# Kernel optimization log

Measured on AMD Instinct MI355X. Metric: run time of the kernel, lower is better.

## Reference

```python
import jax, jax.numpy as jnp
import numpy as np
import math

DIM = 1024; NH = 16; HD = 64; RANK = 512
E = 8; TOPK = 2; EH = 512
THETA = 10000.0; EPS = 1e-6
B = 2; T = 2048


def setup_inputs():
    key = jax.random.key(0)
    ks = jax.random.split(key, 12)
    s = 0.02
    return {
        "x": jax.random.normal(ks[0], (B, T, DIM), jnp.float32),
        "attn_norm_w": jnp.ones((DIM,), jnp.float32),
        "ffn_norm_w": jnp.ones((DIM,), jnp.float32),
        "q_norm_w": jnp.ones((HD,), jnp.float32),
        "k_norm_w": jnp.ones((HD,), jnp.float32),
        "wq": jax.random.normal(ks[1], (NH * HD, DIM), jnp.float32) * s,
        "wkv_down": jax.random.normal(ks[2], (RANK, DIM), jnp.float32) * s,
        "wkv_up": jax.random.normal(ks[3], (2 * NH * HD, RANK), jnp.float32) * s,
        "wo": jax.random.normal(ks[4], (DIM, NH * HD), jnp.float32) * s,
        "gate_w": jax.random.normal(ks[5], (E, DIM), jnp.float32) * s,
        "shared_w1": jax.random.normal(ks[6], (EH, DIM), jnp.float32) * s,
        "shared_w2": jax.random.normal(ks[7], (DIM, EH), jnp.float32) * s,
        "expert_w1": jax.random.normal(ks[8], (E, EH, DIM), jnp.float32) * s,
        "expert_w2": jax.random.normal(ks[9], (E, DIM, EH), jnp.float32) * s,
    }


def rmsnorm(x, w):
    var = jnp.mean(x * x, axis=-1, keepdims=True)
    return x * jax.lax.rsqrt(var + EPS) * w


def rope(x, cos, sin):
    # x: [B,T,H,HD]; pairs are (even, odd) along last dim. cos/sin: [T,1,HD//2]
    xr = x.reshape(*x.shape[:-1], HD // 2, 2)
    a, b = xr[..., 0], xr[..., 1]
    out = jnp.stack([a * cos - b * sin, a * sin + b * cos], axis=-1)
    return out.reshape(x.shape)


def _block(x, attn_norm_w, ffn_norm_w, q_norm_w, k_norm_w,
           wq, wkv_down, wkv_up, wo, gate_w,
           shared_w1, shared_w2, expert_w1, expert_w2):
    Bb, Tt, C = x.shape
    # ---- MLA attention ----
    h_in = rmsnorm(x, attn_norm_w)
    xq = jnp.einsum('btd,ed->bte', h_in, wq).reshape(Bb, Tt, NH, HD)
    latent = jnp.einsum('btd,rd->btr', h_in, wkv_down)
    kv = jnp.einsum('btr,er->bte', latent, wkv_up).reshape(Bb, Tt, 2, NH, HD)
    xk, xv = kv[:, :, 0], kv[:, :, 1]
    xq = rmsnorm(xq, q_norm_w)
    xk = rmsnorm(xk, k_norm_w)
    # RoPE tables
    inv = 1.0 / (THETA ** (jnp.arange(0, HD, 2, dtype=jnp.float32) / HD))  # [HD/2]
    ang = jnp.arange(Tt, dtype=jnp.float32)[:, None] * inv[None, :]       # [T,HD/2]
    cos = jnp.cos(ang)[:, None, :]
    sin = jnp.sin(ang)[:, None, :]
    xq = rope(xq, cos, sin)
    xk = rope(xk, cos, sin)
    scale = 1.0 / math.sqrt(HD)
    scores = jnp.einsum('bqhd,bkhd->bhqk', xq, xk) * scale
    causal = jnp.tril(jnp.ones((Tt, Tt), dtype=bool))
    scores = jnp.where(causal, scores, jnp.finfo(scores.dtype).min)
    attn = jax.nn.softmax(scores, axis=-1)
    attn_out = jnp.einsum('bhqk,bkhd->bqhd', attn, xv).reshape(Bb, Tt, C)
    attn_out = jnp.einsum('bte,de->btd', attn_out, wo)
    h = x + attn_out  # dropout p=0.0 -> identity

    # ---- DeepSeekMoE ----
    xm = rmsnorm(h, ffn_norm_w).reshape(-1, C)  # [N,D]
    shared = jnp.einsum('nh,dh->nd', jax.nn.silu(jnp.einsum('nd,hd->nh', xm, shared_w1)), shared_w2)
    logits = jnp.einsum('nd,ed->ne', xm, gate_w)
    probs = jax.nn.softmax(logits, axis=-1)
    tkw, tki = jax.lax.top_k(probs, TOPK)
    tkw = tkw / jnp.sum(tkw, axis=-1, keepdims=True)
    aux_loss = jnp.sum(jnp.mean(probs, axis=0) * jnp.mean(logits, axis=0)) * E
    # combine weights per expert: [N,E]
    combine = jnp.einsum('nk,nke->ne', tkw, jax.nn.one_hot(tki, E, dtype=tkw.dtype))
    hidden = jax.nn.silu(jnp.einsum('nd,ehd->neh', xm, expert_w1))  # [N,E,EH]
    yexp = jnp.einsum('neh,edh->ned', hidden, expert_w2)            # [N,E,D]
    routed = jnp.einsum('ne,ned->nd', combine, yexp)
    moe_out = (shared + routed).reshape(Bb, Tt, C)
    out = h + moe_out
    return out, aux_loss


def reference(x, attn_norm_w, ffn_norm_w, q_norm_w, k_norm_w,
              wq, wkv_down, wkv_up, wo, gate_w,
              shared_w1, shared_w2, expert_w1, expert_w2):
    return _block(x, attn_norm_w, ffn_norm_w, q_norm_w, k_norm_w,
                  wq, wkv_down, wkv_up, wo, gate_w,
                  shared_w1, shared_w2, expert_w1, expert_w2)
```

## Files before the change

kernel.cpp:

```cpp
#include <hip/hip_runtime.h>
#include <math.h>

#define DIMC 1024
#define NHEADS 16
#define HDC 64
#define RANKC 512
#define NEXP 8
#define EHC 512
#define SEQC 2048
#define NBATCH 2
#define NTOK (NBATCH * SEQC)
#define EPSF 1e-6f

typedef unsigned short u16;
using bf16x8 = __attribute__((ext_vector_type(8))) short;
using f32x4 = __attribute__((ext_vector_type(4))) float;

__device__ inline u16 f2bf(float f) {
    unsigned int u = __float_as_uint(f);
    u += 0x7fff + ((u >> 16) & 1);
    return (u16)(u >> 16);
}
__device__ inline float bf2f(u16 u) { return __uint_as_float(((unsigned int)u) << 16); }

__device__ inline void gld16(const void* g, void* l) {
    __builtin_amdgcn_global_load_lds(
        (const __attribute__((address_space(1))) unsigned int*)g,
        (__attribute__((address_space(3))) unsigned int*)l, 16, 0, 0);
}

__global__ __launch_bounds__(256) void convall_k(
    const float* __restrict__ wq, const float* __restrict__ wkvd,
    const float* __restrict__ wkvu, const float* __restrict__ wo,
    const float* __restrict__ sw1, const float* __restrict__ sw2,
    const float* __restrict__ ew1, const float* __restrict__ ew2,
    u16* __restrict__ wqkvd_h, u16* __restrict__ wqkvd_l,
    u16* __restrict__ wkvu_h, u16* __restrict__ wkvu_l,
    u16* __restrict__ wo_h, u16* __restrict__ wo_l,
    u16* __restrict__ sw1_b, u16* __restrict__ sw2_b,
    u16* __restrict__ ew1_b, u16* __restrict__ ew2_b) {
    size_t f = ((size_t)blockIdx.x * 256 + threadIdx.x) * 4;
    const float* src;
    u16* dh;
    u16* dl = nullptr;
    size_t local;
    if (f < 1048576) { src = wq; dh = wqkvd_h; dl = wqkvd_l; local = f; }
    else if (f < 1572864) { src = wkvd; dh = wqkvd_h + 1048576; dl = wqkvd_l + 1048576; local = f - 1048576; }
    else if (f < 2621440) { src = wkvu; dh = wkvu_h; dl = wkvu_l; local = f - 1572864; }
    else if (f < 3670016) { src = wo; dh = wo_h; dl = wo_l; local = f - 2621440; }
    else if (f < 4194304) { src = sw1; dh = sw1_b; local = f - 3670016; }
    else if (f < 4718592) { src = sw2; dh = sw2_b; local = f - 4194304; }
    else if (f < 8912896) { src = ew1; dh = ew1_b; local = f - 4718592; }
    else { src = ew2; dh = ew2_b; local = f - 8912896; }
    float4 a = *(const float4*)(src + local);
    ushort4 h = make_ushort4(f2bf(a.x), f2bf(a.y), f2bf(a.z), f2bf(a.w));
    *(ushort4*)(dh + local) = h;
    if (dl) {
        ushort4 lo = make_ushort4(f2bf(a.x - bf2f(h.x)), f2bf(a.y - bf2f(h.y)),
                                  f2bf(a.z - bf2f(h.z)), f2bf(a.w - bf2f(h.w)));
        *(ushort4*)(dl + local) = lo;
    }
}

template <bool SPLIT, bool WF32>
__global__ __launch_bounds__(256) void rmsnorm_k(const float* __restrict__ x,
                                                 const float* __restrict__ w,
                                                 u16* __restrict__ oh,
                                                 u16* __restrict__ ol,
                                                 float* __restrict__ of) {
    int row = blockIdx.x;
    const float* xr = x + (size_t)row * DIMC;
    int base = threadIdx.x * 4;
    float4 xv = *(const float4*)(xr + base);
    float ss = xv.x * xv.x + xv.y * xv.y + xv.z * xv.z + xv.w * xv.w;
#pragma unroll
    for (int off = 32; off; off >>= 1) ss += __shfl_down(ss, off);
    __shared__ float sred[4];
    int wid = threadIdx.x >> 6, lane = threadIdx.x & 63;
    if (lane == 0) sred[wid] = ss;
    __syncthreads();
    float tot = sred[0] + sred[1] + sred[2] + sred[3];
    float sc = rsqrtf(tot * (1.0f / DIMC) + EPSF);
    float4 wv = *(const float4*)(w + base);
    float o0 = xv.x * sc * wv.x, o1 = xv.y * sc * wv.y;
    float o2 = xv.z * sc * wv.z, o3 = xv.w * sc * wv.w;
    ushort4 h = make_ushort4(f2bf(o0), f2bf(o1), f2bf(o2), f2bf(o3));
    size_t ob = (size_t)row * DIMC + base;
    *(ushort4*)(oh + ob) = h;
    if (SPLIT) {
        ushort4 lo = make_ushort4(f2bf(o0 - bf2f(h.x)), f2bf(o1 - bf2f(h.y)),
                                  f2bf(o2 - bf2f(h.z)), f2bf(o3 - bf2f(h.w)));
        *(ushort4*)(ol + ob) = lo;
    }
    if (WF32) *(float4*)(of + ob) = make_float4(o0, o1, o2, o3);
}

template <int EPI>
__global__ __launch_bounds__(256) void gemm_sp(const u16* __restrict__ Ah,
                                               const u16* __restrict__ Al,
                                               const u16* __restrict__ Bh,
                                               const u16* __restrict__ Bl,
                                               float* __restrict__ Cf,
                                               u16* __restrict__ Ch,
                                               u16* __restrict__ Cl,
                                               const float* __restrict__ res,
                                               int M, int K) {
    __shared__ u16 AsH[128 * 32], AsL[128 * 32];
    __shared__ u16 BsH[64 * 32], BsL[64 * 32];
    int m0 = blockIdx.x * 64, n0 = blockIdx.y * 128;
    int t = threadIdx.x;
    int w = t >> 6, l = t & 63;
    int wr = w >> 1, wc = w & 1;
    f32x4 acc[4][2];
#pragma unroll
    for (int i = 0; i < 4; i++)
#pragma unroll
        for (int j = 0; j < 2; j++) acc[i][j] = {0.f, 0.f, 0.f, 0.f};
    int lr = t >> 2, lcb = (t & 3) * 8;
    size_t aoff = (size_t)(n0 + lr) * K + lcb;
    size_t boff = (size_t)(m0 + lr) * K + lcb;
    u16* lAH = AsH + t * 8;
    u16* lAL = AsL + t * 8;
    u16* lBH = BsH + t * 8;
    u16* lBL = BsL + t * 8;
    int arow = l & 15, kblk = (l >> 4) * 8;
    for (int k0 = 0; k0 < K; k0 += 32) {
        if (k0) __syncthreads();
        gld16(Ah + aoff + k0, lAH);
        gld16(Ah + aoff + k0 + (size_t)64 * K, lAH + 2048);
        gld16(Al + aoff + k0, lAL);
        gld16(Al + aoff + k0 + (size_t)64 * K, lAL + 2048);
        gld16(Bh + boff + k0, lBH);
        gld16(Bl + boff + k0, lBL);
        __syncthreads();
        bf16x8 ah[4], al[4], bh[2], bl[2];
#pragma unroll
        for (int i = 0; i < 4; i++) {
            int ar = (wr * 64 + i * 16 + arow) * 32 + kblk;
            ah[i] = *(bf16x8*)(AsH + ar);
            al[i] = *(bf16x8*)(AsL + ar);
        }
#pragma unroll
        for (int j = 0; j < 2; j++) {
            int br = (wc * 32 + j * 16 + arow) * 32 + kblk;
            bh[j] = *(bf16x8*)(BsH + br);
            bl[j] = *(bf16x8*)(BsL + br);
        }
#pragma unroll
        for (int i = 0; i < 4; i++)
#pragma unroll
            for (int j = 0; j < 2; j++) {
                acc[i][j] = __builtin_amdgcn_mfma_f32_16x16x32_bf16(ah[i], bh[j], acc[i][j], 0, 0, 0);
                acc[i][j] = __builtin_amdgcn_mfma_f32_16x16x32_bf16(ah[i], bl[j], acc[i][j], 0, 0, 0);
                acc[i][j] = __builtin_amdgcn_mfma_f32_16x16x32_bf16(al[i], bh[j], acc[i][j], 0, 0, 0);
            }
    }
    int crow = (l >> 4) * 4, ccol = l & 15;
#pragma unroll
    for (int i = 0; i < 4; i++) {
#pragma unroll
        for (int r = 0; r < 4; r++) {
            int n = n0 + wr * 64 + i * 16 + crow + r;
#pragma unroll
            for (int j = 0; j < 2; j++) {
                int mc = m0 + wc * 32 + j * 16 + ccol;
                float vv = acc[i][j][r];
                if (EPI == 0 || EPI == 1) {
                    size_t idx = (size_t)n * M + mc;
                    if (EPI == 1) vv += res[idx];
                    Cf[idx] = vv;
                } else {
                    if (mc < 1024) {
                        Cf[(size_t)n * 1024 + mc] = vv;
                    } else {
                        size_t idx = (size_t)n * 512 + (mc - 1024);
                        u16 hi = f2bf(vv);
                        Ch[idx] = hi;
                        Cl[idx] = f2bf(vv - bf2f(hi));
                    }
                }
            }
        }
    }
}

template <int EPI>
__global__ __launch_bounds__(256) void gemm_bf(const u16* __restrict__ A,
                                               const u16* __restrict__ B,
                                               float* __restrict__ Cf,
                                               u16* __restrict__ Cb,
                                               const float* __restrict__ res,
                                               const u16* __restrict__ yx,
                                               const float* __restrict__ tw,
                                               int M, int K) {
    __shared__ u16 As[128 * 32];
    __shared__ u16 Bs[64 * 32];
    int m0 = blockIdx.x * 64, n0 = blockIdx.y * 128;
    int t = threadIdx.x;
    int w = t >> 6, l = t & 63;
    int wr = w >> 1, wc = w & 1;
    f32x4 acc[4][2];
#pragma unroll
    for (int i = 0; i < 4; i++)
#pragma unroll
        for (int j = 0; j < 2; j++) acc[i][j] = {0.f, 0.f, 0.f, 0.f};
    int lr = t >> 2, lcb = (t & 3) * 8;
    const u16* ga = A + (size_t)(n0 + lr) * K + lcb;
    const u16* gb = B + (size_t)(m0 + lr) * K + lcb;
    u16* lA = As + t * 8;
    u16* lB = Bs + t * 8;
    int arow = l & 15, kblk = (l >> 4) * 8;
    for (int k0 = 0; k0 < K; k0 += 32) {
        if (k0) __syncthreads();
        gld16(ga + k0, lA);
        gld16(ga + k0 + (size_t)64 * K, lA + 2048);
        gld16(gb + k0, lB);
        __syncthreads();
        bf16x8 af[4], bfr[2];
#pragma unroll
        for (int i = 0; i < 4; i++)
            af[i] = *(bf16x8*)(As + (wr * 64 + i * 16 + arow) * 32 + kblk);
#pragma unroll
        for (int j = 0; j < 2; j++)
            bfr[j] = *(bf16x8*)(Bs + (wc * 32 + j * 16 + arow) * 32 + kblk);
#pragma unroll
        for (int i = 0; i < 4; i++)
#pragma unroll
            for (int j = 0; j < 2; j++)
                acc[i][j] = __builtin_amdgcn_mfma_f32_16x16x32_bf16(af[i], bfr[j], acc[i][j], 0, 0, 0);
    }
    int crow = (l >> 4) * 4, ccol = l & 15;
#pragma unroll
    for (int i = 0; i < 4; i++) {
#pragma unroll
        for (int r = 0; r < 4; r++) {
            int n = n0 + wr * 64 + i * 16 + crow + r;
#pragma unroll
            for (int j = 0; j < 2; j++) {
                int mc = m0 + wc * 32 + j * 16 + ccol;
                float vv = acc[i][j][r];
                size_t idx = (size_t)n * M + mc;
                if (EPI == 3) {
                    float y0 = bf2f(yx[(size_t)(2 * n) * 1024 + mc]);
                    float y1 = bf2f(yx[(size_t)(2 * n + 1) * 1024 + mc]);
                    Cf[idx] = vv + res[idx] + tw[2 * n] * y0 + tw[2 * n + 1] * y1;
                } else {
                    vv = vv / (1.0f + __expf(-vv));
                    Cb[idx] = f2bf(vv);
                }
            }
        }
    }
}

__global__ __launch_bounds__(256) void qknorm_rope_k(const float* __restrict__ q,
                                                     const float* __restrict__ kv,
                                                     const float* __restrict__ qw,
                                                     const float* __restrict__ kw,
                                                     u16* __restrict__ qhi, u16* __restrict__ qlo,
                                                     u16* __restrict__ khi, u16* __restrict__ klo) {
    int bid = blockIdx.x * 4 + (threadIdx.x >> 6);
    int head = bid & (NHEADS - 1);
    int n = bid >> 4;
    int pos = n & (SEQC - 1);
    int lane = threadIdx.x & 63;
    int i = lane >> 1;
    float inv = powf(10000.0f, -(float)(2 * i) * (1.0f / HDC));
    float ang = (float)pos * inv;
    float cs = cosf(ang), sn = sinf(ang);
    size_t off = (size_t)n * DIMC + head * HDC + lane;
    {
        float v = q[off];
        float ss = v * v;
#pragma unroll
        for (int o2 = 32; o2; o2 >>= 1) ss += __shfl_down(ss, o2);
        ss = __shfl(ss, 0);
        float sc = rsqrtf(ss * (1.0f / HDC) + EPSF);
        v = v * sc * qw[lane];
        float partner = __shfl_xor(v, 1);
        float outv = (lane & 1) ? (partner * sn + v * cs) : (v * cs - partner * sn);
        outv *= 0.125f;
        u16 hi = f2bf(outv);
        qhi[off] = hi;
        qlo[off] = f2bf(outv - bf2f(hi));
    }
    {
        float v = kv[(size_t)n * 2048 + head * HDC + lane];
        float ss = v * v;
#pragma unroll
        for (int o2 = 32; o2; o2 >>= 1) ss += __shfl_down(ss, o2);
        ss = __shfl(ss, 0);
        float sc = rsqrtf(ss * (1.0f / HDC) + EPSF);
        v = v * sc * kw[lane];
        float partner = __shfl_xor(v, 1);
        float outv = (lane & 1) ? (partner * sn + v * cs) : (v * cs - partner * sn);
        u16 hi = f2bf(outv);
        khi[off] = hi;
        klo[off] = f2bf(outv - bf2f(hi));
    }
}

__global__ __launch_bounds__(256) void transp_k(const float* __restrict__ kv,
                                                u16* __restrict__ vthi,
                                                u16* __restrict__ vtlo) {
    __shared__ float T[64][68];
    int j0 = blockIdx.x * 64, head = blockIdx.y, b = blockIdx.z;
    int t = threadIdx.x;
    int jr = t >> 2, c0 = (t & 3) * 16;
    const float* src = kv + ((size_t)(b * SEQC + j0 + jr)) * 2048 + 1024 + head * HDC + c0;
#pragma unroll
    for (int u = 0; u < 4; u++) {
        float4 v4 = *(const float4*)(src + u * 4);
        T[c0 + u * 4 + 0][jr] = v4.x;
        T[c0 + u * 4 + 1][jr] = v4.y;
        T[c0 + u * 4 + 2][jr] = v4.z;
        T[c0 + u * 4 + 3][jr] = v4.w;
    }
    __syncthreads();
    int d = t >> 2, jb = (t & 3) * 16;
    size_t obase = ((size_t)((b * NHEADS + head) * HDC + d)) * SEQC + j0 + jb;
#pragma unroll
    for (int u = 0; u < 4; u++) {
        float f0 = T[d][jb + u * 4 + 0], f1 = T[d][jb + u * 4 + 1];
        float f2 = T[d][jb + u * 4 + 2], f3 = T[d][jb + u * 4 + 3];
        ushort4 h = make_ushort4(f2bf(f0), f2bf(f1), f2bf(f2), f2bf(f3));
        ushort4 lo = make_ushort4(f2bf(f0 - bf2f(h.x)), f2bf(f1 - bf2f(h.y)),
                                  f2bf(f2 - bf2f(h.z)), f2bf(f3 - bf2f(h.w)));
        *(ushort4*)(vthi + obase + u * 4) = h;
        *(ushort4*)(vtlo + obase + u * 4) = lo;
    }
}

__device__ __forceinline__ void attn_tile(const bf16x8 (&qh)[2], const bf16x8 (&ql)[2],
                                          f32x4 (&O)[4], float (&mrow)[4], float (&lrow)[4],
                                          const u16* KHs, const u16* KLs,
                                          const u16* VHs, const u16* VLs,
                                          u16* myPH, u16* myPL,
                                          int la, int lg, int w, bool diag) {
    f32x4 S[4];
    __builtin_amdgcn_s_setprio(1);
#pragma unroll
    for (int ct = 0; ct < 4; ct++) {
        int row = ct * 16 + la;
        int sw = (row & 7) << 4;
        int a0 = ((row << 7) + (lg << 4)) ^ sw;
        int a1 = ((row << 7) + 64 + (lg << 4)) ^ sw;
        bf16x8 kh0 = *(const bf16x8*)((const char*)KHs + a0);
        bf16x8 kh1 = *(const bf16x8*)((const char*)KHs + a1);
        bf16x8 kl0 = *(const bf16x8*)((const char*)KLs + a0);
        bf16x8 kl1 = *(const bf16x8*)((const char*)KLs + a1);
        f32x4 s = {0.f, 0.f, 0.f, 0.f};
        s = __builtin_amdgcn_mfma_f32_16x16x32_bf16(qh[0], kh0, s, 0, 0, 0);
        s = __builtin_amdgcn_mfma_f32_16x16x32_bf16(qh[1], kh1, s, 0, 0, 0);
        s = __builtin_amdgcn_mfma_f32_16x16x32_bf16(qh[0], kl0, s, 0, 0, 0);
        s = __builtin_amdgcn_mfma_f32_16x16x32_bf16(qh[1], kl1, s, 0, 0, 0);
        s = __builtin_amdgcn_mfma_f32_16x16x32_bf16(ql[0], kh0, s, 0, 0, 0);
        s = __builtin_amdgcn_mfma_f32_16x16x32_bf16(ql[1], kh1, s, 0, 0, 0);
        S[ct] = s;
    }
    __builtin_amdgcn_s_setprio(0);
    if (diag) {
#pragma unroll
        for (int ct = 0; ct < 4; ct++)
#pragma unroll
            for (int r = 0; r < 4; r++)
                if (ct * 16 + la > w * 16 + lg * 4 + r) S[ct][r] = -1e30f;
    }
    float rmax[4], rsum[4];
#pragma unroll
    for (int r = 0; r < 4; r++)
        rmax[r] = fmaxf(fmaxf(S[0][r], S[1][r]), fmaxf(S[2][r], S[3][r]));
#pragma unroll
    for (int off = 1; off < 16; off <<= 1)
#pragma unroll
        for (int r = 0; r < 4; r++) rmax[r] = fmaxf(rmax[r], __shfl_xor(rmax[r], off));
    float corr[4];
#pragma unroll
    for (int r = 0; r < 4; r++) {
        float mn = fmaxf(mrow[r], rmax[r]);
        corr[r] = __expf(mrow[r] - mn);
        mrow[r] = mn;
        rsum[r] = 0.f;
    }
#pragma unroll
    for (int ct = 0; ct < 4; ct++) {
#pragma unroll
        for (int r = 0; r < 4; r++) {
            float p = __expf(S[ct][r] - mrow[r]);
            rsum[r] += p;
            u16 hi = f2bf(p);
            int pidx = (lg * 4 + r) * 68 + ct * 16 + la;
            myPH[pidx] = hi;
            myPL[pidx] = f2bf(p - bf2f(hi));
        }
    }
#pragma unroll
    for (int off = 1; off < 16; off <<= 1)
#pragma unroll
        for (int r = 0; r < 4; r++) rsum[r] += __shfl_xor(rsum[r], off);
#pragma unroll
    for (int r = 0; r < 4; r++) lrow[r] = lrow[r] * corr[r] + rsum[r];
#pragma unroll
    for (int ct = 0; ct < 4; ct++)
#pragma unroll
        for (int r = 0; r < 4; r++) O[ct][r] *= corr[r];
    asm volatile("s_waitcnt lgkmcnt(0)" ::: "memory");
    __builtin_amdgcn_sched_barrier(0);
    bf16x8 pa0 = *(const bf16x8*)(myPH + la * 68 + lg * 8);
    bf16x8 pa1 = *(const bf16x8*)(myPH + la * 68 + 32 + lg * 8);
    bf16x8 pl0 = *(const bf16x8*)(myPL + la * 68 + lg * 8);
    bf16x8 pl1 = *(const bf16x8*)(myPL + la * 68 + 32 + lg * 8);
    __builtin_amdgcn_s_setprio(1);
#pragma unroll
    for (int ct = 0; ct < 4; ct++) {
        int row = ct * 16 + la;
        int sw = (row & 7) << 4;
        int a0 = ((row << 7) + (lg << 4)) ^ sw;
        int a1 = ((row << 7) + 64 + (lg << 4)) ^ sw;
        bf16x8 vh0 = *(const bf16x8*)((const char*)VHs + a0);
        bf16x8 vh1 = *(const bf16x8*)((const char*)VHs + a1);
        bf16x8 vl0 = *(const bf16x8*)((const char*)VLs + a0);
        bf16x8 vl1 = *(const bf16x8*)((const char*)VLs + a1);
        f32x4 o = O[ct];
        o = __builtin_amdgcn_mfma_f32_16x16x32_bf16(pa0, vh0, o, 0, 0, 0);
        o = __builtin_amdgcn_mfma_f32_16x16x32_bf16(pa1, vh1, o, 0, 0, 0);
        o = __builtin_amdgcn_mfma_f32_16x16x32_bf16(pl0, vh0, o, 0, 0, 0);
        o = __builtin_amdgcn_mfma_f32_16x16x32_bf16(pl1, vh1, o, 0, 0, 0);
        o = __builtin_amdgcn_mfma_f32_16x16x32_bf16(pa0, vl0, o, 0, 0, 0);
        o = __builtin_amdgcn_mfma_f32_16x16x32_bf16(pa1, vl1, o, 0, 0, 0);
        O[ct] = o;
    }
    __builtin_amdgcn_s_setprio(0);
}

__global__ __launch_bounds__(256) void flash_k(const u16* __restrict__ qhi,
                                               const u16* __restrict__ qlo,
                                               const u16* __restrict__ khi,
                                               const u16* __restrict__ klo,
                                               const u16* __restrict__ vthi,
                                               const u16* __restrict__ vtlo,
                                               u16* __restrict__ aoh,
                                               u16* __restrict__ aol) {
    __shared__ u16 KHs[4096], KLs[4096], VHs[4096], VLs[4096];
    __shared__ u16 PH[4][16 * 68], PL[4][16 * 68];
    int pr = blockIdx.x, head = blockIdx.y, b = blockIdx.z;
    int qtA = pr, qtB = 31 - pr;
    int t = threadIdx.x, w = t >> 6, l = t & 63;
    int la = l & 15, lg = l >> 4;
    size_t qoffA = ((size_t)(b * SEQC + qtA * 64 + w * 16 + la)) * DIMC + head * HDC;
    size_t qoffB = ((size_t)(b * SEQC + qtB * 64 + w * 16 + la)) * DIMC + head * HDC;
    bf16x8 qhA[2], qlA[2], qhB[2], qlB[2];
    qhA[0] = *(const bf16x8*)(qhi + qoffA + lg * 8);
    qhA[1] = *(const bf16x8*)(qhi + qoffA + 32 + lg * 8);
    qlA[0] = *(const bf16x8*)(qlo + qoffA + lg * 8);
    qlA[1] = *(const bf16x8*)(qlo + qoffA + 32 + lg * 8);
    qhB[0] = *(const bf16x8*)(qhi + qoffB + lg * 8);
    qhB[1] = *(const bf16x8*)(qhi + qoffB + 32 + lg * 8);
    qlB[0] = *(const bf16x8*)(qlo + qoffB + lg * 8);
    qlB[1] = *(const bf16x8*)(qlo + qoffB + 32 + lg * 8);
    int d0 = t * 16, d1 = 4096 + t * 16;
    int s0 = d0 ^ (((d0 >> 7) & 7) << 4);
    int s1 = d1 ^ (((d1 >> 7) & 7) << 4);
    int r0 = (s0 >> 7) & 63, ir0 = s0 & 127;
    int r1 = (s1 >> 7) & 63, ir1 = s1 & 127;
    size_t kb0 = ((size_t)(b * SEQC + r0) * DIMC + head * HDC) * 2 + ir0;
    size_t kb1 = ((size_t)(b * SEQC + r1) * DIMC + head * HDC) * 2 + ir1;
    size_t vb0 = ((size_t)((b * NHEADS + head) * HDC + r0)) * SEQC * 2 + ir0;
    size_t vb1 = ((size_t)((b * NHEADS + head) * HDC + r1)) * SEQC * 2 + ir1;
    const char* khp = (const char*)khi;
    const char* klp = (const char*)klo;
    const char* vhp = (const char*)vthi;
    const char* vlp = (const char*)vtlo;
    f32x4 OA[4], OB[4];
#pragma unroll
    for (int ct = 0; ct < 4; ct++) {
        OA[ct] = {0.f, 0.f, 0.f, 0.f};
        OB[ct] = {0.f, 0.f, 0.f, 0.f};
    }
    float mA[4] = {-1e30f, -1e30f, -1e30f, -1e30f};
    float lA[4] = {0.f, 0.f, 0.f, 0.f};
    float mB[4] = {-1e30f, -1e30f, -1e30f, -1e30f};
    float lB[4] = {0.f, 0.f, 0.f, 0.f};
    u16* myPH = PH[w];
    u16* myPL = PL[w];
    for (int kt = 0; kt <= qtB; kt++) {
        __syncthreads();
        size_t ko = (size_t)kt * (64 * DIMC * 2);
        size_t vo = (size_t)kt * 128;
        gld16(khp + kb0 + ko, KHs + t * 8);
        gld16(khp + kb1 + ko, KHs + t * 8 + 2048);
        gld16(klp + kb0 + ko, KLs + t * 8);
        gld16(klp + kb1 + ko, KLs + t * 8 + 2048);
        gld16(vhp + vb0 + vo, VHs + t * 8);
        gld16(vhp + vb1 + vo, VHs + t * 8 + 2048);
        gld16(vlp + vb0 + vo, VLs + t * 8);
        gld16(vlp + vb1 + vo, VLs + t * 8 + 2048);
        __syncthreads();
        attn_tile(qhB, qlB, OB, mB, lB, KHs, KLs, VHs, VLs, myPH, myPL, la, lg, w, kt == qtB);
        if (kt <= qtA)
            attn_tile(qhA, qlA, OA, mA, lA, KHs, KLs, VHs, VLs, myPH, myPL, la, lg, w, kt == qtA);
    }
    size_t obA = ((size_t)(b * SEQC + qtA * 64 + w * 16 + lg * 4)) * DIMC + head * HDC;
    size_t obB = ((size_t)(b * SEQC + qtB * 64 + w * 16 + lg * 4)) * DIMC + head * HDC;
#pragma unroll
    for (int ct = 0; ct < 4; ct++) {
#pragma unroll
        for (int r = 0; r < 4; r++) {
            float va = OA[ct][r] / lA[r];
            size_t ia = obA + (size_t)r * DIMC + ct * 16 + la;
            u16 ha = f2bf(va);
            aoh[ia] = ha;
            aol[ia] = f2bf(va - bf2f(ha));
            float vb = OB[ct][r] / lB[r];
            size_t ib = obB + (size_t)r * DIMC + ct * 16 + la;
            u16 hb = f2bf(vb);
            aoh[ib] = hb;
            aol[ib] = f2bf(vb - bf2f(hb));
        }
    }
}

__global__ __launch_bounds__(256) void gate_k(const float* __restrict__ xm,
                                              const float* __restrict__ gw,
                                              float* __restrict__ topw,
                                              int* __restrict__ topi,
                                              float* __restrict__ plbuf) {
    int w = threadIdx.x >> 6, lane = threadIdx.x & 63;
    int n = blockIdx.x * 4 + w;
    const float* xr = xm + (size_t)n * DIMC;
    float4 xv[4];
#pragma unroll
    for (int c = 0; c < 4; c++) xv[c] = *(const float4*)(xr + c * 256 + lane * 4);
    float acc[NEXP];
#pragma unroll
    for (int e = 0; e < NEXP; e++) {
        const float* gr = gw + (size_t)e * DIMC;
        float a = 0.f;
#pragma unroll
        for (int c = 0; c < 4; c++) {
            float4 gv = *(const float4*)(gr + c * 256 + lane * 4);
            a += xv[c].x * gv.x + xv[c].y * gv.y + xv[c].z * gv.z + xv[c].w * gv.w;
        }
        acc[e] = a;
    }
#pragma unroll
    for (int off = 32; off; off >>= 1)
#pragma unroll
        for (int e = 0; e < NEXP; e++) acc[e] += __shfl_down(acc[e], off);
    if (lane == 0) {
        float lg[NEXP], p[NEXP];
        float mx = -1e30f;
#pragma unroll
        for (int e = 0; e < NEXP; e++) {
            lg[e] = acc[e];
            mx = fmaxf(mx, lg[e]);
        }
        float s = 0.f;
#pragma unroll
        for (int e = 0; e < NEXP; e++) { p[e] = __expf(lg[e] - mx); s += p[e]; }
        float invs = 1.0f / s;
#pragma unroll
        for (int e = 0; e < NEXP; e++) p[e] *= invs;
        int i0 = 0;
        for (int e = 1; e < NEXP; e++) if (p[e] > p[i0]) i0 = e;
        int i1 = (i0 == 0) ? 1 : 0;
        for (int e = 0; e < NEXP; e++) if (e != i0 && p[e] > p[i1]) i1 = e;
        float w0 = p[i0], w1 = p[i1];
        float invw = 1.0f / (w0 + w1);
        topw[n * 2] = w0 * invw;
        topw[n * 2 + 1] = w1 * invw;
        topi[n * 2] = i0;
        topi[n * 2 + 1] = i1;
#pragma unroll
        for (int e = 0; e < NEXP; e++) {
            plbuf[(size_t)e * NTOK + n] = p[e];
            plbuf[(size_t)(NEXP + e) * NTOK + n] = lg[e];
        }
    }
}

__global__ __launch_bounds__(256) void aux_red_k(const float* __restrict__ plbuf,
                                                 float* __restrict__ sums) {
    int col = blockIdx.x;
    const float* src = plbuf + (size_t)col * NTOK;
    float s = 0.f;
#pragma unroll
    for (int i = 0; i < NTOK / 256; i++) s += src[threadIdx.x + i * 256];
#pragma unroll
    for (int off = 32; off; off >>= 1) s += __shfl_down(s, off);
    __shared__ float red[4];
    int wid = threadIdx.x >> 6, lane = threadIdx.x & 63;
    if (lane == 0) red[wid] = s;
    __syncthreads();
    if (threadIdx.x == 0) sums[col] = red[0] + red[1] + red[2] + red[3];
}

__global__ void zero_k(int* cnt) {
    if (threadIdx.x < 8) cnt[threadIdx.x] = 0;
}

__global__ void aux_k(const float* __restrict__ sums, float* __restrict__ out) {
    if (threadIdx.x == 0) {
        const float invN = 1.0f / NTOK;
        float a = 0;
        for (int e = 0; e < NEXP; e++) a += (sums[e] * invN) * (sums[NEXP + e] * invN);
        out[0] = a * NEXP;
    }
}

__global__ __launch_bounds__(256) void route_k(const int* __restrict__ topi,
                                               int* __restrict__ cnt,
                                               int* __restrict__ perm) {
    int n = blockIdx.x * 256 + threadIdx.x;
    if (n >= NTOK) return;
#pragma unroll
    for (int kk = 0; kk < 2; kk++) {
        int slot = n * 2 + kk;
        int e = topi[slot];
        int pos = atomicAdd(&cnt[e], 1);
        perm[e * 4096 + pos] = slot;
    }
}

__global__ __launch_bounds__(256) void moe_h_k(const u16* __restrict__ xb,
                                               const u16* __restrict__ w1,
                                               const int* __restrict__ perm,
                                               const int* __restrict__ cnt,
                                               u16* __restrict__ hid) {
    int e = blockIdx.z;
    int count = cnt[e];
    int n0 = blockIdx.y * 128;
    if (n0 >= count) return;
    int m0 = blockIdx.x * 64;
    __shared__ u16 As[128 * 32];
    __shared__ u16 Bs[64 * 32];
    int t = threadIdx.x;
    int w = t >> 6, l = t & 63;
    int wr = w >> 1, wc = w & 1;
    f32x4 acc[4][2];
#pragma unroll
    for (int i = 0; i < 4; i++)
#pragma unroll
        for (int j = 0; j < 2; j++) acc[i][j] = {0.f, 0.f, 0.f, 0.f};
    int lr = t >> 2, lcb = (t & 3) * 8;
    int tok0 = perm[e * 4096 + min(n0 + lr, count - 1)] >> 1;
    int tok1 = perm[e * 4096 + min(n0 + lr + 64, count - 1)] >> 1;
    const u16* ga0 = xb + (size_t)tok0 * DIMC + lcb;
    const u16* ga1 = xb + (size_t)tok1 * DIMC + lcb;
    const u16* gb = w1 + (size_t)e * EHC * DIMC + (size_t)(m0 + lr) * DIMC + lcb;
    u16* lA = As + t * 8;
    u16* lB = Bs + t * 8;
    int arow = l & 15, kblk = (l >> 4) * 8;
    for (int k0 = 0; k0 < DIMC; k0 += 32) {
        if (k0) __syncthreads();
        gld16(ga0 + k0, lA);
        gld16(ga1 + k0, lA + 2048);
        gld16(gb + k0, lB);
        __syncthreads();
        bf16x8 af[4], bfr[2];
#pragma unroll
        for (int i = 0; i < 4; i++)
            af[i] = *(bf16x8*)(As + (wr * 64 + i * 16 + arow) * 32 + kblk);
#pragma unroll
        for (int j = 0; j < 2; j++)
            bfr[j] = *(bf16x8*)(Bs + (wc * 32 + j * 16 + arow) * 32 + kblk);
#pragma unroll
        for (int i = 0; i < 4; i++)
#pragma unroll
            for (int j = 0; j < 2; j++)
                acc[i][j] = __builtin_amdgcn_mfma_f32_16x16x32_bf16(af[i], bfr[j], acc[i][j], 0, 0, 0);
    }
    int crow = (l >> 4) * 4, ccol = l & 15;
#pragma unroll
    for (int i = 0; i < 4; i++) {
#pragma unroll
        for (int r = 0; r < 4; r++) {
            int hrow = n0 + wr * 64 + i * 16 + crow + r;
            if (hrow >= count) continue;
            int slot = perm[e * 4096 + hrow];
#pragma unroll
            for (int j = 0; j < 2; j++) {
                int mc = m0 + wc * 32 + j * 16 + ccol;
                float vv = acc[i][j][r];
                vv = vv / (1.0f + __expf(-vv));
                hid[(size_t)slot * EHC + mc] = f2bf(vv);
            }
        }
    }
}

__global__ __launch_bounds__(256) void moe_c_k(const u16* __restrict__ hid,
                                               const u16* __restrict__ w2,
                                               const int* __restrict__ perm,
                                               const int* __restrict__ cnt,
                                               u16* __restrict__ yexp) {
    int e = blockIdx.z;
    int count = cnt[e];
    int n0 = blockIdx.y * 128;
    if (n0 >= count) return;
    int m0 = blockIdx.x * 64;
    __shared__ u16 As[128 * 32];
    __shared__ u16 Bs[64 * 32];
    int t = threadIdx.x;
    int w = t >> 6, l = t & 63;
    int wr = w >> 1, wc = w & 1;
    f32x4 acc[4][2];
#pragma unroll
    for (int i = 0; i < 4; i++)
#pragma unroll
        for (int j = 0; j < 2; j++) acc[i][j] = {0.f, 0.f, 0.f, 0.f};
    int lr = t >> 2, lcb = (t & 3) * 8;
    int slot0 = perm[e * 4096 + min(n0 + lr, count - 1)];
    int slot1 = perm[e * 4096 + min(n0 + lr + 64, count - 1)];
    const u16* ga0 = hid + (size_t)slot0 * EHC + lcb;
    const u16* ga1 = hid + (size_t)slot1 * EHC + lcb;
    const u16* gb = w2 + (size_t)e * DIMC * EHC + (size_t)(m0 + lr) * EHC + lcb;
    u16* lA = As + t * 8;
    u16* lB = Bs + t * 8;
    int arow = l & 15, kblk = (l >> 4) * 8;
    for (int k0 = 0; k0 < EHC; k0 += 32) {
        if (k0) __syncthreads();
        gld16(ga0 + k0, lA);
        gld16(ga1 + k0, lA + 2048);
        gld16(gb + k0, lB);
        __syncthreads();
        bf16x8 af[4], bfr[2];
#pragma unroll
        for (int i = 0; i < 4; i++)
            af[i] = *(bf16x8*)(As + (wr * 64 + i * 16 + arow) * 32 + kblk);
#pragma unroll
        for (int j = 0; j < 2; j++)
            bfr[j] = *(bf16x8*)(Bs + (wc * 32 + j * 16 + arow) * 32 + kblk);
#pragma unroll
        for (int i = 0; i < 4; i++)
#pragma unroll
            for (int j = 0; j < 2; j++)
                acc[i][j] = __builtin_amdgcn_mfma_f32_16x16x32_bf16(af[i], bfr[j], acc[i][j], 0, 0, 0);
    }
    int crow = (l >> 4) * 4, ccol = l & 15;
#pragma unroll
    for (int i = 0; i < 4; i++) {
#pragma unroll
        for (int r = 0; r < 4; r++) {
            int pos = n0 + wr * 64 + i * 16 + crow + r;
            if (pos >= count) continue;
            int slot = perm[e * 4096 + pos];
#pragma unroll
            for (int j = 0; j < 2; j++) {
                int mc = m0 + wc * 32 + j * 16 + ccol;
                yexp[(size_t)slot * 1024 + mc] = f2bf(acc[i][j][r]);
            }
        }
    }
}

extern "C" void kernel_launch(void* const* d_in, const int* in_sizes, int n_in,
                              void* d_out, int out_size, void* d_ws, size_t ws_size,
                              hipStream_t stream) {
    const float* x = (const float*)d_in[0];
    const float* attn_nw = (const float*)d_in[1];
    const float* ffn_nw = (const float*)d_in[2];
    const float* q_nw = (const float*)d_in[3];
    const float* k_nw = (const float*)d_in[4];
    const float* wq = (const float*)d_in[5];
    const float* wkv_down = (const float*)d_in[6];
    const float* wkv_up = (const float*)d_in[7];
    const float* wo = (const float*)d_in[8];
    const float* gate_w = (const float*)d_in[9];
    const float* sw1 = (const float*)d_in[10];
    const float* sw2 = (const float*)d_in[11];
    const float* ew1 = (const float*)d_in[12];
    const float* ew2 = (const float*)d_in[13];
    float* out = (float*)d_out;
    char* W = (char*)d_ws;
    const size_t MB = (size_t)1 << 20;

    u16* wqkvd_h = (u16*)(W + 0 * MB);
    u16* wqkvd_l = (u16*)(W + 3 * MB);
    u16* wkvu_h = (u16*)(W + 6 * MB);
    u16* wkvu_l = (u16*)(W + 8 * MB);
    u16* wo_h = (u16*)(W + 10 * MB);
    u16* wo_l = (u16*)(W + 12 * MB);
    u16* sw1_b = (u16*)(W + 14 * MB);
    u16* sw2_b = (u16*)(W + 15 * MB);
    u16* ew1_b = (u16*)(W + 16 * MB);
    u16* ew2_b = (u16*)(W + 24 * MB);
    u16* hin_h = (u16*)(W + 32 * MB);
    u16* hin_l = (u16*)(W + 40 * MB);
    float* qf = (float*)(W + 48 * MB);
    float* kvf = (float*)(W + 64 * MB);
    u16* lat_h = (u16*)(W + 96 * MB);
    u16* lat_l = (u16*)(W + 100 * MB);
    u16* qhi = (u16*)(W + 104 * MB);
    u16* qlo = (u16*)(W + 112 * MB);
    u16* khi = (u16*)(W + 120 * MB);
    u16* klo = (u16*)(W + 128 * MB);
    u16* vthi = (u16*)(W + 136 * MB);
    u16* vtlo = (u16*)(W + 144 * MB);
    float* sums = (float*)(W + 152 * MB);
    int* cnt = (int*)(W + 152 * MB + 256);
    float* topw = (float*)(W + 152 * MB + 4096);
    int* topi = (int*)(W + 152 * MB + 4096 + 32768);
    int* perm = (int*)(W + 152 * MB + 4096 + 65536);
    float* plbuf = (float*)(W + 153 * MB);
    u16* ao_h = hin_h;
    u16* ao_l = hin_l;
    u16* xm_b = (u16*)qf;
    float* h = (float*)(W + 64 * MB);
    float* xm_f = (float*)(W + 80 * MB);
    u16* s1_b = lat_h;
    u16* hid = qhi;
    u16* yexp = qlo;

    convall_k<<<12800, 256, 0, stream>>>(wq, wkv_down, wkv_up, wo, sw1, sw2, ew1, ew2,
                                         wqkvd_h, wqkvd_l, wkvu_h, wkvu_l,
                                         wo_h, wo_l, sw1_b, sw2_b, ew1_b, ew2_b);

    rmsnorm_k<true, false><<<NTOK, 256, 0, stream>>>(x, attn_nw, hin_h, hin_l, nullptr);
    gemm_sp<5><<<dim3(24, 32), 256, 0, stream>>>(hin_h, hin_l, wqkvd_h, wqkvd_l, qf, lat_h, lat_l, nullptr, 1024, DIMC);
    gemm_sp<0><<<dim3(32, 32), 256, 0, stream>>>(lat_h, lat_l, wkvu_h, wkvu_l, kvf, nullptr, nullptr, nullptr, 2048, RANKC);
    qknorm_rope_k<<<NTOK * NHEADS / 4, 256, 0, stream>>>(qf, kvf, q_nw, k_nw, qhi, qlo, khi, klo);
    transp_k<<<dim3(SEQC / 64, NHEADS, NBATCH), 256, 0, stream>>>(kvf, vthi, vtlo);
    flash_k<<<dim3(16, NHEADS, NBATCH), 256, 0, stream>>>(qhi, qlo, khi, klo, vthi, vtlo, ao_h, ao_l);
    gemm_sp<1><<<dim3(16, 32), 256, 0, stream>>>(ao_h, ao_l, wo_h, wo_l, h, nullptr, nullptr, x, DIMC, DIMC);
    rmsnorm_k<false, true><<<NTOK, 256, 0, stream>>>(h, ffn_nw, xm_b, nullptr, xm_f);
    zero_k<<<1, 64, 0, stream>>>(cnt);
    gate_k<<<NTOK / 4, 256, 0, stream>>>(xm_f, gate_w, topw, topi, plbuf);
    aux_red_k<<<16, 256, 0, stream>>>(plbuf, sums);
    route_k<<<16, 256, 0, stream>>>(topi, cnt, perm);
    gemm_bf<2><<<dim3(8, 32), 256, 0, stream>>>(xm_b, sw1_b, nullptr, s1_b, nullptr, nullptr, nullptr, EHC, DIMC);
    moe_h_k<<<dim3(8, 32, 8), 256, 0, stream>>>(xm_b, ew1_b, perm, cnt, hid);
    moe_c_k<<<dim3(16, 32, 8), 256, 0, stream>>>(hid, ew2_b, perm, cnt, yexp);
    gemm_bf<3><<<dim3(16, 32), 256, 0, stream>>>(s1_b, sw2_b, out, nullptr, h, yexp, topw, DIMC, EHC);
    aux_k<<<1, 64, 0, stream>>>(sums, out + 4194304);
}
```

Before: 472.8 us.

## Fuse ffn rmsnorm with gating, merge shared-expert GEMM into MoE, remap flash grid

The FFN RMSNorm now computes the gate logits, softmax and top-2 in the same kernel. This removes the fp32 normalized-activation write and the separate gate kernel's reread. The shared-expert first GEMM runs as a ninth z-slice of the routed expert up-projection launch, which saves a launch and lets the two overlap. The flash attention grid is flattened to 1D with an XCD-aware remap of block index to (pair, head, batch), intended to improve L2 locality of K/V across blocks on the same XCD.

Measured after the change: 452.2 us. 4.3% less time.

```diff
diff --git a/kernel.cpp b/kernel.cpp
--- a/kernel.cpp
+++ b/kernel.cpp
@@ -62,12 +62,11 @@
     }
 }
 
-template <bool SPLIT, bool WF32>
+template <bool SPLIT>
 __global__ __launch_bounds__(256) void rmsnorm_k(const float* __restrict__ x,
                                                  const float* __restrict__ w,
                                                  u16* __restrict__ oh,
-                                                 u16* __restrict__ ol,
-                                                 float* __restrict__ of) {
+                                                 u16* __restrict__ ol) {
     int row = blockIdx.x;
     const float* xr = x + (size_t)row * DIMC;
     int base = threadIdx.x * 4;
@@ -92,7 +91,78 @@
                                   f2bf(o2 - bf2f(h.z)), f2bf(o3 - bf2f(h.w)));
         *(ushort4*)(ol + ob) = lo;
     }
-    if (WF32) *(float4*)(of + ob) = make_float4(o0, o1, o2, o3);
+}
+
+__global__ __launch_bounds__(256) void rmsnorm_gate_k(const float* __restrict__ x,
+                                                      const float* __restrict__ w,
+                                                      u16* __restrict__ oh,
+                                                      const float* __restrict__ gw,
+                                                      float* __restrict__ topw,
+                                                      int* __restrict__ topi,
+                                                      float* __restrict__ plbuf) {
+    int row = blockIdx.x;
+    const float* xr = x + (size_t)row * DIMC;
+    int base = threadIdx.x * 4;
+    float4 xv = *(const float4*)(xr + base);
+    float ss = xv.x * xv.x + xv.y * xv.y + xv.z * xv.z + xv.w * xv.w;
+#pragma unroll
+    for (int off = 32; off; off >>= 1) ss += __shfl_down(ss, off);
+    __shared__ float sred[4];
+    __shared__ float red[4][NEXP];
+    int wid = threadIdx.x >> 6, lane = threadIdx.x & 63;
+    if (lane == 0) sred[wid] = ss;
+    __syncthreads();
+    float tot = sred[0] + sred[1] + sred[2] + sred[3];
+    float sc = rsqrtf(tot * (1.0f / DIMC) + EPSF);
+    float4 wv = *(const float4*)(w + base);
+    float o0 = xv.x * sc * wv.x, o1 = xv.y * sc * wv.y;
+    float o2 = xv.z * sc * wv.z, o3 = xv.w * sc * wv.w;
+    size_t ob = (size_t)row * DIMC + base;
+    *(ushort4*)(oh + ob) = make_ushort4(f2bf(o0), f2bf(o1), f2bf(o2), f2bf(o3));
+    float acc[NEXP];
+#pragma unroll
+    for (int e = 0; e < NEXP; e++) {
+        float4 gv = *(const float4*)(gw + (size_t)e * DIMC + base);
+        acc[e] = o0 * gv.x + o1 * gv.y + o2 * gv.z + o3 * gv.w;
+    }
+#pragma unroll
+    for (int off = 32; off; off >>= 1)
+#pragma unroll
+        for (int e = 0; e < NEXP; e++) acc[e] += __shfl_down(acc[e], off);
+    if (lane == 0)
+#pragma unroll
+        for (int e = 0; e < NEXP; e++) red[wid][e] = acc[e];
+    __syncthreads();
+    if (threadIdx.x == 0) {
+        float lg[NEXP], p[NEXP];
+        float mx = -1e30f;
+#pragma unroll
+        for (int e = 0; e < NEXP; e++) {
+            lg[e] = red[0][e] + red[1][e] + red[2][e] + red[3][e];
+            mx = fmaxf(mx, lg[e]);
+        }
+        float s = 0.f;
+#pragma unroll
+        for (int e = 0; e < NEXP; e++) { p[e] = __expf(lg[e] - mx); s += p[e]; }
+        float invs = 1.0f / s;
+#pragma unroll
+        for (int e = 0; e < NEXP; e++) p[e] *= invs;
+        int i0 = 0;
+        for (int e = 1; e < NEXP; e++) if (p[e] > p[i0]) i0 = e;
+        int i1 = (i0 == 0) ? 1 : 0;
+        for (int e = 0; e < NEXP; e++) if (e != i0 && p[e] > p[i1]) i1 = e;
+        float w0 = p[i0], w1 = p[i1];
+        float invw = 1.0f / (w0 + w1);
+        topw[row * 2] = w0 * invw;
+        topw[row * 2 + 1] = w1 * invw;
+        topi[row * 2] = i0;
+        topi[row * 2 + 1] = i1;
+#pragma unroll
+        for (int e = 0; e < NEXP; e++) {
+            plbuf[(size_t)e * NTOK + row] = p[e];
+            plbuf[(size_t)(NEXP + e) * NTOK + row] = lg[e];
+        }
+    }
 }
 
 template <int EPI>
@@ -184,15 +254,13 @@
     }
 }
 
-template <int EPI>
-__global__ __launch_bounds__(256) void gemm_bf(const u16* __restrict__ A,
-                                               const u16* __restrict__ B,
-                                               float* __restrict__ Cf,
-                                               u16* __restrict__ Cb,
-                                               const float* __restrict__ res,
-                                               const u16* __restrict__ yx,
-                                               const float* __restrict__ tw,
-                                               int M, int K) {
+__global__ __launch_bounds__(256) void gemm_fin(const u16* __restrict__ A,
+                                                const u16* __restrict__ B,
+                                                float* __restrict__ Cf,
+                                                const float* __restrict__ res,
+                                                const u16* __restrict__ yx,
+                                                const float* __restrict__ tw,
+                                                int M, int K) {
     __shared__ u16 As[128 * 32];
     __shared__ u16 Bs[64 * 32];
     int m0 = blockIdx.x * 64, n0 = blockIdx.y * 128;
@@ -238,16 +306,10 @@
 #pragma unroll
             for (int j = 0; j < 2; j++) {
                 int mc = m0 + wc * 32 + j * 16 + ccol;
-                float vv = acc[i][j][r];
                 size_t idx = (size_t)n * M + mc;
-                if (EPI == 3) {
-                    float y0 = bf2f(yx[(size_t)(2 * n) * 1024 + mc]);
-                    float y1 = bf2f(yx[(size_t)(2 * n + 1) * 1024 + mc]);
-                    Cf[idx] = vv + res[idx] + tw[2 * n] * y0 + tw[2 * n + 1] * y1;
-                } else {
-                    vv = vv / (1.0f + __expf(-vv));
-                    Cb[idx] = f2bf(vv);
-                }
+                float y0 = bf2f(yx[(size_t)(2 * n) * 1024 + mc]);
+                float y1 = bf2f(yx[(size_t)(2 * n + 1) * 1024 + mc]);
+                Cf[idx] = acc[i][j][r] + res[idx] + tw[2 * n] * y0 + tw[2 * n + 1] * y1;
             }
         }
     }
@@ -443,7 +505,11 @@
                                                u16* __restrict__ aol) {
     __shared__ u16 KHs[4096], KLs[4096], VHs[4096], VLs[4096];
     __shared__ u16 PH[4][16 * 68], PL[4][16 * 68];
-    int pr = blockIdx.x, head = blockIdx.y, b = blockIdx.z;
+    int id = blockIdx.x;
+    int xcd = id & 7, slot = id >> 3;
+    int grp = ((slot >> 4) << 3) | xcd;
+    int pr = slot & 15;
+    int head = grp & 15, b = grp >> 4;
     int qtA = pr, qtB = 31 - pr;
     int t = threadIdx.x, w = t >> 6, l = t & 63;
     int la = l & 15, lg = l >> 4;
@@ -520,65 +586,6 @@
     }
 }
 
-__global__ __launch_bounds__(256) void gate_k(const float* __restrict__ xm,
-                                              const float* __restrict__ gw,
-                                              float* __restrict__ topw,
-                                              int* __restrict__ topi,
-                                              float* __restrict__ plbuf) {
-    int w = threadIdx.x >> 6, lane = threadIdx.x & 63;
-    int n = blockIdx.x * 4 + w;
-    const float* xr = xm + (size_t)n * DIMC;
-    float4 xv[4];
-#pragma unroll
-    for (int c = 0; c < 4; c++) xv[c] = *(const float4*)(xr + c * 256 + lane * 4);
-    float acc[NEXP];
-#pragma unroll
-    for (int e = 0; e < NEXP; e++) {
-        const float* gr = gw + (size_t)e * DIMC;
-        float a = 0.f;
-#pragma unroll
-        for (int c = 0; c < 4; c++) {
-            float4 gv = *(const float4*)(gr + c * 256 + lane * 4);
-            a += xv[c].x * gv.x + xv[c].y * gv.y + xv[c].z * gv.z + xv[c].w * gv.w;
-        }
-        acc[e] = a;
-    }
-#pragma unroll
-    for (int off = 32; off; off >>= 1)
-#pragma unroll
-        for (int e = 0; e < NEXP; e++) acc[e] += __shfl_down(acc[e], off);
-    if (lane == 0) {
-        float lg[NEXP], p[NEXP];
-        float mx = -1e30f;
-#pragma unroll
-        for (int e = 0; e < NEXP; e++) {
-            lg[e] = acc[e];
-            mx = fmaxf(mx, lg[e]);
-        }
-        float s = 0.f;
-#pragma unroll
-        for (int e = 0; e < NEXP; e++) { p[e] = __expf(lg[e] - mx); s += p[e]; }
-        float invs = 1.0f / s;
-#pragma unroll
-        for (int e = 0; e < NEXP; e++) p[e] *= invs;
-        int i0 = 0;
-        for (int e = 1; e < NEXP; e++) if (p[e] > p[i0]) i0 = e;
-        int i1 = (i0 == 0) ? 1 : 0;
-        for (int e = 0; e < NEXP; e++) if (e != i0 && p[e] > p[i1]) i1 = e;
-        float w0 = p[i0], w1 = p[i1];
-        float invw = 1.0f / (w0 + w1);
-        topw[n * 2] = w0 * invw;
-        topw[n * 2 + 1] = w1 * invw;
-        topi[n * 2] = i0;
-        topi[n * 2 + 1] = i1;
-#pragma unroll
-        for (int e = 0; e < NEXP; e++) {
-            plbuf[(size_t)e * NTOK + n] = p[e];
-            plbuf[(size_t)(NEXP + e) * NTOK + n] = lg[e];
-        }
-    }
-}
-
 __global__ __launch_bounds__(256) void aux_red_k(const float* __restrict__ plbuf,
                                                  float* __restrict__ sums) {
     int col = blockIdx.x;
@@ -624,11 +631,14 @@
 
 __global__ __launch_bounds__(256) void moe_h_k(const u16* __restrict__ xb,
                                                const u16* __restrict__ w1,
+                                               const u16* __restrict__ sw1b,
                                                const int* __restrict__ perm,
                                                const int* __restrict__ cnt,
-                                               u16* __restrict__ hid) {
+                                               u16* __restrict__ hid,
+                                               u16* __restrict__ s1b) {
     int e = blockIdx.z;
-    int count = cnt[e];
+    bool shared = (e == NEXP);
+    int count = shared ? NTOK : cnt[e];
     int n0 = blockIdx.y * 128;
     if (n0 >= count) return;
     int m0 = blockIdx.x * 64;
@@ -643,11 +653,17 @@
 #pragma unroll
         for (int j = 0; j < 2; j++) acc[i][j] = {0.f, 0.f, 0.f, 0.f};
     int lr = t >> 2, lcb = (t & 3) * 8;
-    int tok0 = perm[e * 4096 + min(n0 + lr, count - 1)] >> 1;
-    int tok1 = perm[e * 4096 + min(n0 + lr + 64, count - 1)] >> 1;
+    int tok0, tok1;
+    if (shared) {
+        tok0 = n0 + lr;
+        tok1 = n0 + lr + 64;
+    } else {
+        tok0 = perm[e * 4096 + min(n0 + lr, count - 1)] >> 1;
+        tok1 = perm[e * 4096 + min(n0 + lr + 64, count - 1)] >> 1;
+    }
     const u16* ga0 = xb + (size_t)tok0 * DIMC + lcb;
     const u16* ga1 = xb + (size_t)tok1 * DIMC + lcb;
-    const u16* gb = w1 + (size_t)e * EHC * DIMC + (size_t)(m0 + lr) * DIMC + lcb;
+    const u16* gb = (shared ? sw1b : w1 + (size_t)e * EHC * DIMC) + (size_t)(m0 + lr) * DIMC + lcb;
     u16* lA = As + t * 8;
     u16* lB = Bs + t * 8;
     int arow = l & 15, kblk = (l >> 4) * 8;
@@ -677,13 +693,14 @@
         for (int r = 0; r < 4; r++) {
             int hrow = n0 + wr * 64 + i * 16 + crow + r;
             if (hrow >= count) continue;
-            int slot = perm[e * 4096 + hrow];
+            size_t dstrow = shared ? (size_t)hrow : (size_t)perm[e * 4096 + hrow];
+            u16* dst = shared ? s1b : hid;
 #pragma unroll
             for (int j = 0; j < 2; j++) {
                 int mc = m0 + wc * 32 + j * 16 + ccol;
                 float vv = acc[i][j][r];
                 vv = vv / (1.0f + __expf(-vv));
-                hid[(size_t)slot * EHC + mc] = f2bf(vv);
+                dst[dstrow * EHC + mc] = f2bf(vv);
             }
         }
     }
@@ -807,7 +824,6 @@
     u16* ao_l = hin_l;
     u16* xm_b = (u16*)qf;
     float* h = (float*)(W + 64 * MB);
-    float* xm_f = (float*)(W + 80 * MB);
     u16* s1_b = lat_h;
     u16* hid = qhi;
     u16* yexp = qlo;
@@ -816,21 +832,19 @@
                                          wqkvd_h, wqkvd_l, wkvu_h, wkvu_l,
                                          wo_h, wo_l, sw1_b, sw2_b, ew1_b, ew2_b);
 
-    rmsnorm_k<true, false><<<NTOK, 256, 0, stream>>>(x, attn_nw, hin_h, hin_l, nullptr);
+    rmsnorm_k<true><<<NTOK, 256, 0, stream>>>(x, attn_nw, hin_h, hin_l);
     gemm_sp<5><<<dim3(24, 32), 256, 0, stream>>>(hin_h, hin_l, wqkvd_h, wqkvd_l, qf, lat_h, lat_l, nullptr, 1024, DIMC);
     gemm_sp<0><<<dim3(32, 32), 256, 0, stream>>>(lat_h, lat_l, wkvu_h, wkvu_l, kvf, nullptr, nullptr, nullptr, 2048, RANKC);
     qknorm_rope_k<<<NTOK * NHEADS / 4, 256, 0, stream>>>(qf, kvf, q_nw, k_nw, qhi, qlo, khi, klo);
     transp_k<<<dim3(SEQC / 64, NHEADS, NBATCH), 256, 0, stream>>>(kvf, vthi, vtlo);
-    flash_k<<<dim3(16, NHEADS, NBATCH), 256, 0, stream>>>(qhi, qlo, khi, klo, vthi, vtlo, ao_h, ao_l);
+    flash_k<<<dim3(512), 256, 0, stream>>>(qhi, qlo, khi, klo, vthi, vtlo, ao_h, ao_l);
     gemm_sp<1><<<dim3(16, 32), 256, 0, stream>>>(ao_h, ao_l, wo_h, wo_l, h, nullptr, nullptr, x, DIMC, DIMC);
-    rmsnorm_k<false, true><<<NTOK, 256, 0, stream>>>(h, ffn_nw, xm_b, nullptr, xm_f);
     zero_k<<<1, 64, 0, stream>>>(cnt);
-    gate_k<<<NTOK / 4, 256, 0, stream>>>(xm_f, gate_w, topw, topi, plbuf);
+    rmsnorm_gate_k<<<NTOK, 256, 0, stream>>>(h, ffn_nw, xm_b, gate_w, topw, topi, plbuf);
     aux_red_k<<<16, 256, 0, stream>>>(plbuf, sums);
     route_k<<<16, 256, 0, stream>>>(topi, cnt, perm);
-    gemm_bf<2><<<dim3(8, 32), 256, 0, stream>>>(xm_b, sw1_b, nullptr, s1_b, nullptr, nullptr, nullptr, EHC, DIMC);
-    moe_h_k<<<dim3(8, 32, 8), 256, 0, stream>>>(xm_b, ew1_b, perm, cnt, hid);
+    moe_h_k<<<dim3(8, 32, 9), 256, 0, stream>>>(xm_b, ew1_b, sw1_b, perm, cnt, hid, s1_b);
     moe_c_k<<<dim3(16, 32, 8), 256, 0, stream>>>(hid, ew2_b, perm, cnt, yexp);
-    gemm_bf<3><<<dim3(16, 32), 256, 0, stream>>>(s1_b, sw2_b, out, nullptr, h, yexp, topw, DIMC, EHC);
+    gemm_fin<<<dim3(16, 32), 256, 0, stream>>>(s1_b, sw2_b, out, h, yexp, topw, DIMC, EHC);
     aux_k<<<1, 64, 0, stream>>>(sums, out + 4194304);
 }
```
